# Optimization experiments

Measured on AMD Instinct MI355X. Metric: run time of the kernel, lower is better.

The kernel has to match this reference:

```python
import jax, jax.numpy as jnp
from jax import lax
import numpy as np

B, T = 256, 1024
LSTM_DIMS = [(64, 128), (256, 128), (256, 64)]  # (input, hidden) per layer


def setup_inputs() -> dict:
    key = jax.random.key(0)
    ks = jax.random.split(key, 32)
    s = 0.05
    p = {}
    p["x"] = jax.random.normal(ks[0], (B, 1, T), jnp.float32)
    p["conv_w"] = jax.random.normal(ks[1], (64, 1, 5), jnp.float32) * s  # OIW
    p["conv_b"] = jnp.zeros((64,), jnp.float32)
    for i, (D, H) in enumerate(LSTM_DIMS, 1):
        p[f"w_ih{i}"] = jax.random.normal(ks[3 * i], (2, 4 * H, D), jnp.float32) * s  # [dir, 4H, D]
        p[f"w_hh{i}"] = jax.random.normal(ks[3 * i + 1], (2, 4 * H, H), jnp.float32) * s
        p[f"b{i}"] = jnp.zeros((2, 4 * H), jnp.float32)  # b_ih + b_hh combined (equivalent math)
    fc_dims = [(512, 128), (256, 512), (128, 256), (2, 128)]
    for j, (O, I) in enumerate(fc_dims, 1):
        p[f"fc{j}_w"] = jax.random.normal(ks[12 + 2 * j], (O, I), jnp.float32) * s
        p[f"fc{j}_b"] = jnp.zeros((O,), jnp.float32)
    return p


def _lstm_dir(x, w_ih, w_hh, b, reverse):
    # x: [B,T,D] -> h: [B,T,H]; PyTorch gate order i,f,g,o
    Hh = w_hh.shape[1]
    xs = jnp.swapaxes(x, 0, 1)  # [T,B,D]
    if reverse:
        xs = xs[::-1]
    xw = jnp.einsum('tbd,gd->tbg', xs, w_ih) + b  # precompute input GEMMs: [T,B,4H]

    def step(carry, xw_t):
        h, c = carry
        gates = xw_t + h @ w_hh.T
        i, f, g, o = jnp.split(gates, 4, axis=-1)
        c = jax.nn.sigmoid(f) * c + jax.nn.sigmoid(i) * jnp.tanh(g)
        h = jax.nn.sigmoid(o) * jnp.tanh(c)
        return (h, c), h

    Bx = x.shape[0]
    init = (jnp.zeros((Bx, Hh), x.dtype), jnp.zeros((Bx, Hh), x.dtype))
    _, hs = lax.scan(step, init, xw)
    if reverse:
        hs = hs[::-1]
    return jnp.swapaxes(hs, 0, 1)  # [B,T,H]


def _bilstm(x, w_ih, w_hh, b):
    hf = _lstm_dir(x, w_ih[0], w_hh[0], b[0], False)
    hb = _lstm_dir(x, w_ih[1], w_hh[1], b[1], True)
    return jnp.concatenate([hf, hb], axis=-1)


def reference(x, conv_w, conv_b, w_ih1, w_hh1, b1, w_ih2, w_hh2, b2,
              w_ih3, w_hh3, b3, fc1_w, fc1_b, fc2_w, fc2_b, fc3_w, fc3_b, fc4_w, fc4_b):
    # causal conv: left-pad (k-1)=4, then VALID conv
    xp = jnp.pad(x, ((0, 0), (0, 0), (4, 0)))
    y = lax.conv_general_dilated(xp, conv_w, (1,), 'VALID',
                                 dimension_numbers=('NCH', 'OIH', 'NCH'))
    y = jax.nn.relu(y + conv_b[None, :, None]).transpose(0, 2, 1)  # [B,T,64]
    y = _bilstm(y, w_ih1, w_hh1, b1)  # [B,T,256]
    y = _bilstm(y, w_ih2, w_hh2, b2)  # [B,T,256]
    y = _bilstm(y, w_ih3, w_hh3, b3)  # [B,T,128]
    h = y[:, -1, :]  # [B,128]
    h = jax.nn.relu(h @ fc1_w.T + fc1_b)
    h = jax.nn.relu(h @ fc2_w.T + fc2_b)
    h = jax.nn.relu(h @ fc3_w.T + fc3_b)
    return h @ fc4_w.T + fc4_b  # [B,2]
```

## Files before the change

### kernel.cpp

```cpp
#include <hip/hip_runtime.h>
#include <hip/hip_bf16.h>
#include <cstdint>
#include <cstddef>

#define B_ALL 256
#define T_SZ  1024

typedef __attribute__((ext_vector_type(8))) _Float16  halfx8;
typedef __attribute__((ext_vector_type(4))) _Float16  halfx4;
typedef __attribute__((ext_vector_type(4))) float     f32x4;

__device__ __forceinline__ float sig_(float x) {
    return __builtin_amdgcn_rcpf(1.0f + __expf(-x));
}
__device__ __forceinline__ float tanh_(float x) {
    float ax = fabsf(x);
    float e  = __expf(-2.0f * ax);
    float t  = (1.0f - e) * __builtin_amdgcn_rcpf(1.0f + e);
    return copysignf(t, x);
}

__device__ __forceinline__ void bar_lgkm() {
    asm volatile("s_waitcnt lgkmcnt(0)\n\ts_barrier" ::: "memory");
}

__global__ void conv_relu_kernel(const float* __restrict__ x, const float* __restrict__ w,
                                 const float* __restrict__ bias, _Float16* __restrict__ out,
                                 int bg0)
{
    int c  = threadIdx.x & 63;
    int tq = threadIdx.x >> 6;
    int t  = blockIdx.x * 4 + tq;
    int b  = blockIdx.y;
    const float* xb = x + (size_t)(bg0 + b) * T_SZ;
    float s = bias[c];
#pragma unroll
    for (int k = 0; k < 5; ++k) {
        int ti = t - 4 + k;
        float xv = (ti >= 0) ? xb[ti] : 0.0f;
        s = fmaf(w[c * 5 + k], xv, s);
    }
    out[((size_t)b * T_SZ + t) * 64 + c] = (_Float16)fmaxf(s, 0.0f);
}

template <int H, int NW, bool WRITE_Y>
__global__ __launch_bounds__(512, 1) void fused_step(
    const _Float16* __restrict__ xwR, const float* __restrict__ w_hh,
    _Float16* __restrict__ y, float* __restrict__ lastOut,
    float* __restrict__ Hst, float* __restrict__ Cst,
    int Bg, int Tc, int lg, int step0, int zeroInit, int writeLast,
    int nRecBlocks, int ndirRec,
    const _Float16* __restrict__ A, const float* __restrict__ W,
    const float* __restrict__ bias, _Float16* __restrict__ xwOut,
    int K, int N, int t0p, int MT, int NT)
{
    __shared__ __align__(16) char smem[32768];
    const int tid = threadIdx.x;
    const int w   = tid >> 6;
    const int l   = tid & 63;
    const int l15 = l & 15;
    const int q4  = l >> 4;

    if ((int)blockIdx.x < nRecBlocks) {
        constexpr int FH  = 4 * H;
        constexpr int KT  = H / 32;
        constexpr int NCH = H / 8;
        int rb  = blockIdx.x;
        int dir = (ndirRec == 2) ? (rb & 1) : 0;
        int bt  = (ndirRec == 2) ? (rb >> 1) : rb;
        int brow = bt * 4 + q4;
        int hh   = w * 16 + l15;

        _Float16* hb = (_Float16*)smem;
        auto hAddr = [&](int p, int row, int ch) -> _Float16* {
            return hb + ((((p * 16 + row) * NCH) + (ch ^ (row & (NCH - 1)))) << 3);
        };
        for (int i = tid; i < 2 * 16 * NCH * 8; i += 512) hb[i] = (_Float16)0.f;
        __syncthreads();

        halfx8 wf[4][KT];
        float creg = 0.f;
        if (w < NW) {
            const float* wbase = w_hh + (size_t)dir * FH * H;
#pragma unroll
            for (int gate = 0; gate < 4; ++gate) {
                const float* wrow = wbase + (size_t)(gate * H + hh) * H;
#pragma unroll
                for (int kt = 0; kt < KT; ++kt) {
                    const float* src = wrow + kt * 32 + q4 * 8;
                    float4 a = *(const float4*)(src);
                    float4 b = *(const float4*)(src + 4);
                    halfx8 v;
                    v[0] = (_Float16)a.x; v[1] = (_Float16)a.y; v[2] = (_Float16)a.z; v[3] = (_Float16)a.w;
                    v[4] = (_Float16)b.x; v[5] = (_Float16)b.y; v[6] = (_Float16)b.z; v[7] = (_Float16)b.w;
                    wf[gate][kt] = v;
                }
            }
            float hv = 0.f;
            if (!zeroInit) {
                hv   = Hst[((size_t)dir * Bg + brow) * H + hh];
                creg = Cst[((size_t)dir * Bg + brow) * H + hh];
            }
            hAddr(0, q4 * 4, hh >> 3)[hh & 7] = (_Float16)hv;
        }
        const _Float16* xb = xwR + (size_t)dir * Tc * Bg * FH + (size_t)brow * FH + hh * 4;
        const size_t xstride = (size_t)Bg * FH;

        halfx4 pf0, pf1, pf2, pf3;
        if (w < NW) {
            pf0 = *(const halfx4*)(xb);
            pf1 = *(const halfx4*)(xb + xstride);
            pf2 = *(const halfx4*)(xb + 2 * xstride);
            pf3 = *(const halfx4*)(xb + 3 * xstride);
        }
        __syncthreads();

        auto step = [&](int sl, int P, halfx4 xv) {
            const int t = dir ? (T_SZ - 1 - (step0 + sl)) : (step0 + sl);
            halfx8 af[KT];
#pragma unroll
            for (int kt = 0; kt < KT; ++kt)
                af[kt] = *(const halfx8*)hAddr(P, l15, kt * 4 + q4);
            float g4[4];
#pragma unroll
            for (int gate = 0; gate < 4; ++gate) {
                f32x4 a = {0.f, 0.f, 0.f, 0.f};
#pragma unroll
                for (int kt = 0; kt < KT; ++kt)
                    a = __builtin_amdgcn_mfma_f32_16x16x32_f16(af[kt], wf[gate][kt], a, 0, 0, 0);
                g4[gate] = a[0] + (float)xv[gate];
            }
            float iv = fminf(fmaxf(g4[0], -25.f), 25.f);
            float fv = fminf(fmaxf(g4[1], -25.f), 25.f);
            float gv = fminf(fmaxf(g4[2], -12.f), 12.f);
            float ov = fminf(fmaxf(g4[3], -25.f), 25.f);
            float Af = 1.f + __expf(-fv);
            float Bi = 1.f + __expf(-iv);
            float G  = __expf(2.f * gv);
            float Gp = G + 1.f, Gm = G - 1.f;
            float num = fmaf(creg * Bi, Gp, Af * Gm);
            float cn  = num * __builtin_amdgcn_rcpf(Af * Bi * Gp);
            creg = cn;
            float cc = fminf(fmaxf(cn, -25.f), 25.f);
            float E  = __expf(2.f * cc);
            float hv = (E - 1.f) * __builtin_amdgcn_rcpf((1.f + __expf(-ov)) * (E + 1.f));
            hAddr(1 - P, q4 * 4, hh >> 3)[hh & 7] = (_Float16)hv;
            if (WRITE_Y) {
                y[((size_t)brow * T_SZ + t) * (2 * H) + dir * H + hh] = (_Float16)hv;
            } else if (writeLast && sl == Tc - 1) {
                lastOut[brow * 128 + hh] = hv;
            }
            if (sl == Tc - 1) {
                Hst[((size_t)dir * Bg + brow) * H + hh] = hv;
                Cst[((size_t)dir * Bg + brow) * H + hh] = cn;
            }
        };

        for (int sl4 = 0; sl4 < Tc; sl4 += 4) {
            if (w < NW) {
                step(sl4 + 0, 0, pf0);
                if (sl4 + 4 < Tc) pf0 = *(const halfx4*)(xb + (size_t)(sl4 + 4) * xstride);
            }
            bar_lgkm();
            if (w < NW) {
                step(sl4 + 1, 1, pf1);
                if (sl4 + 5 < Tc) pf1 = *(const halfx4*)(xb + (size_t)(sl4 + 5) * xstride);
            }
            bar_lgkm();
            if (w < NW) {
                step(sl4 + 2, 0, pf2);
                if (sl4 + 6 < Tc) pf2 = *(const halfx4*)(xb + (size_t)(sl4 + 6) * xstride);
            }
            bar_lgkm();
            if (w < NW) {
                step(sl4 + 3, 1, pf3);
                if (sl4 + 7 < Tc) pf3 = *(const halfx4*)(xb + (size_t)(sl4 + 7) * xstride);
            }
            bar_lgkm();
        }
    } else {
        const int Tcp = 1 << lg;
        const int H4  = N >> 2;
        int pb   = blockIdx.x - nRecBlocks;
        int mi   = pb % MT;
        int rest = pb / MT;
        int ni   = rest % NT;
        int dir  = rest / NT;
        const float* Wd = W + (size_t)dir * N * K;
        const float* bd = bias + (size_t)dir * N;
        _Float16*    od = xwOut + (size_t)dir * Tcp * Bg * N;

        _Float16 (*As)[40] = (_Float16(*)[40])smem;
        _Float16 (*Ws)[40] = (_Float16(*)[40])(smem + 10240);

        const int m0 = mi * 128;
        const int n0 = ni * 128;
        const int wm = (w & 1) * 64;
        const int wn = (w >> 1) * 32;

        f32x4 acc[4][2];
#pragma unroll
        for (int i = 0; i < 4; i++)
#pragma unroll
            for (int j = 0; j < 2; j++) acc[i][j] = (f32x4){0.f, 0.f, 0.f, 0.f};

        for (int k0 = 0; k0 < K; k0 += 32) {
            {
                int row = tid >> 2;
                int ko  = (tid & 3) * 8;
                int m   = m0 + row;
                int bA  = m >> lg, tl = m & (Tcp - 1);
                int t   = dir ? (T_SZ - 1 - (t0p + tl)) : (t0p + tl);
                const _Float16* src = A + ((size_t)bA * T_SZ + t) * K + k0 + ko;
                *(halfx8*)&As[row][ko] = *(const halfx8*)src;
            }
#pragma unroll
            for (int pass = 0; pass < 2; ++pass) {
                int c2  = tid + pass * 512;
                int row = c2 >> 3;
                int ko  = (c2 & 7) * 4;
                int n_o = n0 + row;
                int nr  = (n_o & 3) * H4 + (n_o >> 2);
                float4 f = *(const float4*)&Wd[(size_t)nr * K + k0 + ko];
                halfx4 v;
                v[0] = (_Float16)f.x; v[1] = (_Float16)f.y; v[2] = (_Float16)f.z; v[3] = (_Float16)f.w;
                *(halfx4*)&Ws[row][ko] = v;
            }
            bar_lgkm();
            halfx8 af[4], bfr[2];
#pragma unroll
            for (int i = 0; i < 4; i++) af[i]  = *(const halfx8*)&As[wm + i * 16 + l15][q4 * 8];
#pragma unroll
            for (int j = 0; j < 2; j++) bfr[j] = *(const halfx8*)&Ws[wn + j * 16 + l15][q4 * 8];
#pragma unroll
            for (int i = 0; i < 4; i++)
#pragma unroll
                for (int j = 0; j < 2; j++)
                    acc[i][j] = __builtin_amdgcn_mfma_f32_16x16x32_f16(af[i], bfr[j], acc[i][j], 0, 0, 0);
            bar_lgkm();
        }

        _Float16 (*Ct)[128] = (_Float16(*)[128])smem;
#pragma unroll
        for (int i = 0; i < 4; i++) {
#pragma unroll
            for (int j = 0; j < 2; j++) {
                int o_l = wn + j * 16 + l15;
                int n_o = n0 + o_l;
                float bi = bd[(n_o & 3) * H4 + (n_o >> 2)];
#pragma unroll
                for (int r = 0; r < 4; r++)
                    Ct[wm + i * 16 + q4 * 4 + r][o_l] = (_Float16)(acc[i][j][r] + bi);
            }
        }
        bar_lgkm();
        {
            int row = tid >> 2;
            int seg = tid & 3;
            int m   = m0 + row;
            int bO  = m >> lg, tl = m & (Tcp - 1);
            _Float16* dst = od + ((size_t)tl * Bg + bO) * N + n0 + seg * 32;
            const _Float16* srcp = &Ct[row][seg * 32];
#pragma unroll
            for (int u = 0; u < 4; ++u)
                *(halfx8*)(dst + u * 8) = *(const halfx8*)(srcp + u * 8);
        }
    }
}

__global__ __launch_bounds__(256) void lstm3_bwd_kernel(
    const _Float16* __restrict__ y2, const float* __restrict__ w_ih3,
    const float* __restrict__ b3, float* __restrict__ H3)
{
    int b = blockIdx.x, g = threadIdx.x;
    __shared__ float xr[256];
    __shared__ float gsh[256];
    xr[g] = (float)y2[((size_t)b * T_SZ + (T_SZ - 1)) * 256 + g];
    __syncthreads();
    const float* wr = w_ih3 + (size_t)256 * 256 + (size_t)g * 256;
    float acc = b3[256 + g];
#pragma unroll 4
    for (int k = 0; k < 256; k++) acc = fmaf(wr[k], xr[k], acc);
    gsh[g] = acc;
    __syncthreads();
    if (g < 64) {
        float iv = gsh[g], gv = gsh[128 + g], ov = gsh[192 + g];
        float ct = sig_(iv) * tanh_(gv);
        float hv = sig_(ov) * tanh_(ct);
        H3[b * 128 + 64 + g] = hv;
    }
}

__global__ void fc_kernel(const float* __restrict__ in, const float* __restrict__ W,
                          const float* __restrict__ bias, float* __restrict__ out,
                          int K, int N, int doRelu)
{
    int b = blockIdx.x;
    int g = threadIdx.x;
    extern __shared__ float xr[];
    for (int i = g; i < K; i += blockDim.x) xr[i] = in[(size_t)b * K + i];
    __syncthreads();
    if (g < N) {
        const float* wr = W + (size_t)g * K;
        float acc = bias[g];
        for (int k = 0; k < K; k++) acc = fmaf(wr[k], xr[k], acc);
        if (doRelu) acc = fmaxf(acc, 0.f);
        out[(size_t)b * N + g] = acc;
    }
}

extern "C" void kernel_launch(void* const* d_in, const int* in_sizes, int n_in,
                              void* d_out, int out_size, void* d_ws, size_t ws_size,
                              hipStream_t stream)
{
    (void)in_sizes; (void)n_in; (void)out_size;
    const float* x      = (const float*)d_in[0];
    const float* conv_w = (const float*)d_in[1];
    const float* conv_b = (const float*)d_in[2];
    const float* w_ih1  = (const float*)d_in[3];
    const float* w_hh1  = (const float*)d_in[4];
    const float* b1     = (const float*)d_in[5];
    const float* w_ih2  = (const float*)d_in[6];
    const float* w_hh2  = (const float*)d_in[7];
    const float* b2     = (const float*)d_in[8];
    const float* w_ih3  = (const float*)d_in[9];
    const float* w_hh3  = (const float*)d_in[10];
    const float* b3     = (const float*)d_in[11];
    const float* fc1_w  = (const float*)d_in[12];
    const float* fc1_b  = (const float*)d_in[13];
    const float* fc2_w  = (const float*)d_in[14];
    const float* fc2_b  = (const float*)d_in[15];
    const float* fc3_w  = (const float*)d_in[16];
    const float* fc3_b  = (const float*)d_in[17];
    const float* fc4_w  = (const float*)d_in[18];
    const float* fc4_b  = (const float*)d_in[19];
    float* out = (float*)d_out;
    char*  base = (char*)d_ws;

    const size_t MB = 1ull << 20;

    auto need = [&](int s, int tc) -> size_t {
        size_t Bg = B_ALL / s;
        size_t YB = Bg * T_SZ * 256 * 2;
        size_t XW = (size_t)tc * Bg * 512 * 2 * 2;
        return 2 * YB + 2 * XW + 2 * MB;
    };

    int S = 8;
    for (int s : {1, 2, 4, 8}) {
        if (need(s, 32) <= ws_size) { S = s; break; }
    }
    int Tc = 32;
    while (Tc < 256 && need(S, Tc * 2) <= ws_size) Tc <<= 1;
    int lg = 0; while ((1 << lg) < Tc) lg++;
    int NC = T_SZ / Tc;

    int Bg = B_ALL / S;
    size_t YB  = (size_t)Bg * T_SZ * 256 * 2;
    size_t XWB = (size_t)Tc * Bg * 512 * 2 * 2;
    _Float16* Y1 = (_Float16*)base;
    _Float16* Y2 = (_Float16*)(base + YB);
    _Float16* X1 = Y2;
    _Float16* XW[2] = { (_Float16*)(base + 2 * YB), (_Float16*)(base + 2 * YB + XWB) };
    float* sm  = (float*)(base + 2 * YB + 2 * XWB);
    float* Hs = sm;
    float* Cs = Hs + 2 * Bg * 128;
    float* H3 = Cs + 2 * Bg * 128;
    float* F1 = H3 + Bg * 128;
    float* F2 = F1 + Bg * 512;
    float* F3 = F2 + Bg * 256;

    int MT = Bg * Tc / 128;

    for (int sp = 0; sp < S; ++sp) {
        int bg0 = sp * Bg;

        conv_relu_kernel<<<dim3(T_SZ / 4, Bg), 256, 0, stream>>>(x, conv_w, conv_b, X1, bg0);

        {
            int NT = 4, ndir = 2, Kl = 64, Nn = 512;
            int nProj = MT * NT * ndir, nRec = (Bg / 4) * ndir;
            fused_step<128, 8, true><<<nProj, 512, 0, stream>>>(
                XW[0], w_hh1, Y1, H3, Hs, Cs, Bg, Tc, lg, 0, 1, 0, 0, ndir,
                X1, w_ih1, b1, XW[0], Kl, Nn, 0, MT, NT);
            int par = 0;
            for (int ci = 0; ci < NC; ++ci) {
                int last = (ci == NC - 1);
                int grid = nRec + (last ? 0 : nProj);
                fused_step<128, 8, true><<<grid, 512, 0, stream>>>(
                    XW[par], w_hh1, Y1, H3, Hs, Cs, Bg, Tc, lg, ci * Tc, ci == 0, 0, nRec, ndir,
                    X1, w_ih1, b1, XW[1 - par], Kl, Nn, (ci + 1) * Tc, MT, NT);
                par ^= 1;
            }
        }
        {
            int NT = 4, ndir = 2, Kl = 256, Nn = 512;
            int nProj = MT * NT * ndir, nRec = (Bg / 4) * ndir;
            fused_step<128, 8, true><<<nProj, 512, 0, stream>>>(
                XW[0], w_hh2, Y2, H3, Hs, Cs, Bg, Tc, lg, 0, 1, 0, 0, ndir,
                Y1, w_ih2, b2, XW[0], Kl, Nn, 0, MT, NT);
            int par = 0;
            for (int ci = 0; ci < NC; ++ci) {
                int last = (ci == NC - 1);
                int grid = nRec + (last ? 0 : nProj);
                fused_step<128, 8, true><<<grid, 512, 0, stream>>>(
                    XW[par], w_hh2, Y2, H3, Hs, Cs, Bg, Tc, lg, ci * Tc, ci == 0, 0, nRec, ndir,
                    Y1, w_ih2, b2, XW[1 - par], Kl, Nn, (ci + 1) * Tc, MT, NT);
                par ^= 1;
            }
        }
        {
            int NT = 2, ndir = 1, Kl = 256, Nn = 256;
            int nProj = MT * NT * ndir, nRec = (Bg / 4) * ndir;
            fused_step<64, 4, false><<<nProj, 512, 0, stream>>>(
                XW[0], w_hh3, nullptr, H3, Hs, Cs, Bg, Tc, lg, 0, 1, 0, 0, ndir,
                Y2, w_ih3, b3, XW[0], Kl, Nn, 0, MT, NT);
            int par = 0;
            for (int ci = 0; ci < NC; ++ci) {
                int last = (ci == NC - 1);
                int grid = nRec + (last ? 0 : nProj);
                fused_step<64, 4, false><<<grid, 512, 0, stream>>>(
                    XW[par], w_hh3, nullptr, H3, Hs, Cs, Bg, Tc, lg, ci * Tc, ci == 0, last, nRec, ndir,
                    Y2, w_ih3, b3, XW[1 - par], Kl, Nn, (ci + 1) * Tc, MT, NT);
                par ^= 1;
            }
        }
        lstm3_bwd_kernel<<<Bg, 256, 0, stream>>>(Y2, w_ih3, b3, H3);

        fc_kernel<<<Bg, 512, 128 * 4, stream>>>(H3, fc1_w, fc1_b, F1, 128, 512, 1);
        fc_kernel<<<Bg, 256, 512 * 4, stream>>>(F1, fc2_w, fc2_b, F2, 512, 256, 1);
        fc_kernel<<<Bg, 128, 256 * 4, stream>>>(F2, fc3_w, fc3_b, F3, 256, 128, 1);
        fc_kernel<<<Bg, 64, 128 * 4, stream>>>(F3, fc4_w, fc4_b, out + (size_t)bg0 * 2, 128, 2, 0);
    }
}
```

Before: 3.674 ms.

## Use full 16-row MFMA tiles per recurrent block and persist projection blocks

Each recurrent block now handles 16 batch rows instead of 4, using all four rows of each MFMA accumulator. Previously only one accumulator element per lane was used, so three quarters of the MFMA output was discarded. This cuts recurrent block count by four. Projection GEMM blocks become persistent and loop over tiles, with the grid sized so recurrent plus projection blocks total 256, roughly one per CU. The trade-off is more pointwise gate work and more xw prefetch registers per lane, and fewer recurrent blocks running in parallel.

```diff
diff --git a/kernel.cpp b/kernel.cpp
--- a/kernel.cpp
+++ b/kernel.cpp
@@ -43,7 +43,58 @@
     out[((size_t)b * T_SZ + t) * 64 + c] = (_Float16)fmaxf(s, 0.0f);
 }
 
-template <int H, int NW, bool WRITE_Y>
+#define REC_STEP(SL, PP, JJ) do {                                                          \
+    const int t_ = dir ? (T_SZ - 1 - (step0 + (SL))) : (step0 + (SL));                     \
+    halfx8 af[KT];                                                                          \
+    _Pragma("unroll")                                                                       \
+    for (int kt = 0; kt < KT; ++kt)                                                         \
+        af[kt] = *(const halfx8*)hAddr((PP), l15, kt * 4 + q4);                             \
+    f32x4 acc_[4];                                                                          \
+    _Pragma("unroll")                                                                       \
+    for (int g_ = 0; g_ < 4; ++g_) {                                                        \
+        f32x4 a_ = {0.f, 0.f, 0.f, 0.f};                                                    \
+        _Pragma("unroll")                                                                   \
+        for (int kt = 0; kt < KT; ++kt)                                                     \
+            a_ = __builtin_amdgcn_mfma_f32_16x16x32_f16(af[kt], wf[g_][kt], a_, 0, 0, 0);   \
+        acc_[g_] = a_;                                                                      \
+    }                                                                                       \
+    _Pragma("unroll")                                                                       \
+    for (int r_ = 0; r_ < 4; ++r_) {                                                        \
+        int m_ = q4 * 4 + r_;                                                               \
+        int brow_ = b0 + m_;                                                                \
+        halfx4 xv_ = pf[(JJ)][r_];                                                          \
+        float iv = acc_[0][r_] + (float)xv_[0];                                             \
+        float fv = acc_[1][r_] + (float)xv_[1];                                             \
+        float gv = acc_[2][r_] + (float)xv_[2];                                             \
+        float ov = acc_[3][r_] + (float)xv_[3];                                             \
+        iv = fminf(fmaxf(iv, -25.f), 25.f);                                                 \
+        fv = fminf(fmaxf(fv, -25.f), 25.f);                                                 \
+        gv = fminf(fmaxf(gv, -12.f), 12.f);                                                 \
+        ov = fminf(fmaxf(ov, -25.f), 25.f);                                                 \
+        float Af = 1.f + __expf(-fv);                                                       \
+        float Bi = 1.f + __expf(-iv);                                                       \
+        float G  = __expf(2.f * gv);                                                        \
+        float Gp = G + 1.f, Gm = G - 1.f;                                                   \
+        float num = fmaf(creg[r_] * Bi, Gp, Af * Gm);                                       \
+        float cn  = num * __builtin_amdgcn_rcpf(Af * Bi * Gp);                              \
+        creg[r_] = cn;                                                                      \
+        float cc = fminf(fmaxf(cn, -25.f), 25.f);                                           \
+        float E  = __expf(2.f * cc);                                                        \
+        float hvv = (E - 1.f) * __builtin_amdgcn_rcpf((1.f + __expf(-ov)) * (E + 1.f));     \
+        hAddr(1 - (PP), m_, hh >> 3)[hh & 7] = (_Float16)hvv;                               \
+        if (WRITE_Y) {                                                                      \
+            y[((size_t)brow_ * T_SZ + t_) * (2 * H) + dir * H + hh] = (_Float16)hvv;        \
+        } else if (writeLast && (SL) == Tc - 1) {                                           \
+            lastOut[brow_ * 128 + hh] = hvv;                                                \
+        }                                                                                   \
+        if ((SL) == Tc - 1) {                                                               \
+            Hst[((size_t)dir * Bg + brow_) * H + hh] = hvv;                                 \
+            Cst[((size_t)dir * Bg + brow_) * H + hh] = cn;                                  \
+        }                                                                                   \
+    }                                                                                       \
+} while (0)
+
+template <int H, bool WRITE_Y>
 __global__ __launch_bounds__(512, 1) void fused_step(
     const _Float16* __restrict__ xwR, const float* __restrict__ w_hh,
     _Float16* __restrict__ y, float* __restrict__ lastOut,
@@ -52,7 +103,7 @@
     int nRecBlocks, int ndirRec,
     const _Float16* __restrict__ A, const float* __restrict__ W,
     const float* __restrict__ bias, _Float16* __restrict__ xwOut,
-    int K, int N, int t0p, int MT, int NT)
+    int K, int N, int t0p, int MT, int NT, int nProjB, int totTiles)
 {
     __shared__ __align__(16) char smem[32768];
     const int tid = threadIdx.x;
@@ -64,22 +115,23 @@
     if ((int)blockIdx.x < nRecBlocks) {
         constexpr int FH  = 4 * H;
         constexpr int KT  = H / 32;
+        constexpr int NW  = H / 16;
         constexpr int NCH = H / 8;
         int rb  = blockIdx.x;
         int dir = (ndirRec == 2) ? (rb & 1) : 0;
         int bt  = (ndirRec == 2) ? (rb >> 1) : rb;
-        int brow = bt * 4 + q4;
-        int hh   = w * 16 + l15;
+        int b0  = bt * 16;
+        int hh  = w * 16 + l15;
 
         _Float16* hb = (_Float16*)smem;
         auto hAddr = [&](int p, int row, int ch) -> _Float16* {
             return hb + ((((p * 16 + row) * NCH) + (ch ^ (row & (NCH - 1)))) << 3);
         };
-        for (int i = tid; i < 2 * 16 * NCH * 8; i += 512) hb[i] = (_Float16)0.f;
+        for (int i = tid; i < 2 * 16 * H; i += 512) hb[i] = (_Float16)0.f;
         __syncthreads();
 
         halfx8 wf[4][KT];
-        float creg = 0.f;
+        float creg[4] = {0.f, 0.f, 0.f, 0.f};
         if (w < NW) {
             const float* wbase = w_hh + (size_t)dir * FH * H;
 #pragma unroll
@@ -96,174 +148,160 @@
                     wf[gate][kt] = v;
                 }
             }
-            float hv = 0.f;
-            if (!zeroInit) {
-                hv   = Hst[((size_t)dir * Bg + brow) * H + hh];
-                creg = Cst[((size_t)dir * Bg + brow) * H + hh];
-            }
-            hAddr(0, q4 * 4, hh >> 3)[hh & 7] = (_Float16)hv;
-        }
-        const _Float16* xb = xwR + (size_t)dir * Tc * Bg * FH + (size_t)brow * FH + hh * 4;
-        const size_t xstride = (size_t)Bg * FH;
-
-        halfx4 pf0, pf1, pf2, pf3;
+#pragma unroll
+            for (int r = 0; r < 4; ++r) {
+                int m = q4 * 4 + r;
+                int brow = b0 + m;
+                float hv = 0.f, cv = 0.f;
+                if (!zeroInit) {
+                    hv = Hst[((size_t)dir * Bg + brow) * H + hh];
+                    cv = Cst[((size_t)dir * Bg + brow) * H + hh];
+                }
+                creg[r] = cv;
+                hAddr(0, m, hh >> 3)[hh & 7] = (_Float16)hv;
+            }
+        }
+        const _Float16* xb = xwR + (size_t)dir * Tc * Bg * FH + (size_t)b0 * FH + hh * 4;
+        const size_t xstr = (size_t)Bg * FH;
+
+        halfx4 pf[4][4];
         if (w < NW) {
-            pf0 = *(const halfx4*)(xb);
-            pf1 = *(const halfx4*)(xb + xstride);
-            pf2 = *(const halfx4*)(xb + 2 * xstride);
-            pf3 = *(const halfx4*)(xb + 3 * xstride);
+#pragma unroll
+            for (int j = 0; j < 4; ++j)
+#pragma unroll
+                for (int r = 0; r < 4; ++r)
+                    pf[j][r] = *(const halfx4*)(xb + (size_t)j * xstr + (q4 * 4 + r) * FH);
         }
         __syncthreads();
-
-        auto step = [&](int sl, int P, halfx4 xv) {
-            const int t = dir ? (T_SZ - 1 - (step0 + sl)) : (step0 + sl);
-            halfx8 af[KT];
-#pragma unroll
-            for (int kt = 0; kt < KT; ++kt)
-                af[kt] = *(const halfx8*)hAddr(P, l15, kt * 4 + q4);
-            float g4[4];
-#pragma unroll
-            for (int gate = 0; gate < 4; ++gate) {
-                f32x4 a = {0.f, 0.f, 0.f, 0.f};
-#pragma unroll
-                for (int kt = 0; kt < KT; ++kt)
-                    a = __builtin_amdgcn_mfma_f32_16x16x32_f16(af[kt], wf[gate][kt], a, 0, 0, 0);
-                g4[gate] = a[0] + (float)xv[gate];
-            }
-            float iv = fminf(fmaxf(g4[0], -25.f), 25.f);
-            float fv = fminf(fmaxf(g4[1], -25.f), 25.f);
-            float gv = fminf(fmaxf(g4[2], -12.f), 12.f);
-            float ov = fminf(fmaxf(g4[3], -25.f), 25.f);
-            float Af = 1.f + __expf(-fv);
-            float Bi = 1.f + __expf(-iv);
-            float G  = __expf(2.f * gv);
-            float Gp = G + 1.f, Gm = G - 1.f;
-            float num = fmaf(creg * Bi, Gp, Af * Gm);
-            float cn  = num * __builtin_amdgcn_rcpf(Af * Bi * Gp);
-            creg = cn;
-            float cc = fminf(fmaxf(cn, -25.f), 25.f);
-            float E  = __expf(2.f * cc);
-            float hv = (E - 1.f) * __builtin_amdgcn_rcpf((1.f + __expf(-ov)) * (E + 1.f));
-            hAddr(1 - P, q4 * 4, hh >> 3)[hh & 7] = (_Float16)hv;
-            if (WRITE_Y) {
-                y[((size_t)brow * T_SZ + t) * (2 * H) + dir * H + hh] = (_Float16)hv;
-            } else if (writeLast && sl == Tc - 1) {
-                lastOut[brow * 128 + hh] = hv;
-            }
-            if (sl == Tc - 1) {
-                Hst[((size_t)dir * Bg + brow) * H + hh] = hv;
-                Cst[((size_t)dir * Bg + brow) * H + hh] = cn;
-            }
-        };
 
         for (int sl4 = 0; sl4 < Tc; sl4 += 4) {
             if (w < NW) {
-                step(sl4 + 0, 0, pf0);
-                if (sl4 + 4 < Tc) pf0 = *(const halfx4*)(xb + (size_t)(sl4 + 4) * xstride);
+                REC_STEP(sl4 + 0, 0, 0);
+                if (sl4 + 4 < Tc) {
+#pragma unroll
+                    for (int r = 0; r < 4; ++r)
+                        pf[0][r] = *(const halfx4*)(xb + (size_t)(sl4 + 4) * xstr + (q4 * 4 + r) * FH);
+                }
             }
             bar_lgkm();
             if (w < NW) {
-                step(sl4 + 1, 1, pf1);
-                if (sl4 + 5 < Tc) pf1 = *(const halfx4*)(xb + (size_t)(sl4 + 5) * xstride);
+                REC_STEP(sl4 + 1, 1, 1);
+                if (sl4 + 5 < Tc) {
+#pragma unroll
+                    for (int r = 0; r < 4; ++r)
+                        pf[1][r] = *(const halfx4*)(xb + (size_t)(sl4 + 5) * xstr + (q4 * 4 + r) * FH);
+                }
             }
             bar_lgkm();
             if (w < NW) {
-                step(sl4 + 2, 0, pf2);
-                if (sl4 + 6 < Tc) pf2 = *(const halfx4*)(xb + (size_t)(sl4 + 6) * xstride);
+                REC_STEP(sl4 + 2, 0, 2);
+                if (sl4 + 6 < Tc) {
+#pragma unroll
+                    for (int r = 0; r < 4; ++r)
+                        pf[2][r] = *(const halfx4*)(xb + (size_t)(sl4 + 6) * xstr + (q4 * 4 + r) * FH);
+                }
             }
             bar_lgkm();
             if (w < NW) {
-                step(sl4 + 3, 1, pf3);
-                if (sl4 + 7 < Tc) pf3 = *(const halfx4*)(xb + (size_t)(sl4 + 7) * xstride);
+                REC_STEP(sl4 + 3, 1, 3);
+                if (sl4 + 7 < Tc) {
+#pragma unroll
+                    for (int r = 0; r < 4; ++r)
+                        pf[3][r] = *(const halfx4*)(xb + (size_t)(sl4 + 7) * xstr + (q4 * 4 + r) * FH);
+                }
             }
             bar_lgkm();
         }
     } else {
         const int Tcp = 1 << lg;
         const int H4  = N >> 2;
-        int pb   = blockIdx.x - nRecBlocks;
-        int mi   = pb % MT;
-        int rest = pb / MT;
-        int ni   = rest % NT;
-        int dir  = rest / NT;
-        const float* Wd = W + (size_t)dir * N * K;
-        const float* bd = bias + (size_t)dir * N;
-        _Float16*    od = xwOut + (size_t)dir * Tcp * Bg * N;
-
-        _Float16 (*As)[40] = (_Float16(*)[40])smem;
-        _Float16 (*Ws)[40] = (_Float16(*)[40])(smem + 10240);
-
-        const int m0 = mi * 128;
-        const int n0 = ni * 128;
-        const int wm = (w & 1) * 64;
-        const int wn = (w >> 1) * 32;
-
-        f32x4 acc[4][2];
-#pragma unroll
-        for (int i = 0; i < 4; i++)
-#pragma unroll
-            for (int j = 0; j < 2; j++) acc[i][j] = (f32x4){0.f, 0.f, 0.f, 0.f};
-
-        for (int k0 = 0; k0 < K; k0 += 32) {
+        int pb = blockIdx.x - nRecBlocks;
+
+        for (int tile = pb; tile < totTiles; tile += nProjB) {
+            int mi   = tile % MT;
+            int rest = tile / MT;
+            int ni   = rest % NT;
+            int dirp = rest / NT;
+            const float* Wd = W + (size_t)dirp * N * K;
+            const float* bd = bias + (size_t)dirp * N;
+            _Float16*    od = xwOut + (size_t)dirp * Tcp * Bg * N;
+
+            _Float16 (*As)[40] = (_Float16(*)[40])smem;
+            _Float16 (*Ws)[40] = (_Float16(*)[40])(smem + 10240);
+
+            const int m0 = mi * 128;
+            const int n0 = ni * 128;
+            const int wm = (w & 1) * 64;
+            const int wn = (w >> 1) * 32;
+
+            f32x4 acc[4][2];
+#pragma unroll
+            for (int i = 0; i < 4; i++)
+#pragma unroll
+                for (int j = 0; j < 2; j++) acc[i][j] = (f32x4){0.f, 0.f, 0.f, 0.f};
+
+            for (int k0 = 0; k0 < K; k0 += 32) {
+                {
+                    int row = tid >> 2;
+                    int ko  = (tid & 3) * 8;
+                    int m   = m0 + row;
+                    int bA  = m >> lg, tl = m & (Tcp - 1);
+                    int t   = dirp ? (T_SZ - 1 - (t0p + tl)) : (t0p + tl);
+                    const _Float16* src = A + ((size_t)bA * T_SZ + t) * K + k0 + ko;
+                    *(halfx8*)&As[row][ko] = *(const halfx8*)src;
+                }
+#pragma unroll
+                for (int pass = 0; pass < 2; ++pass) {
+                    int c2  = tid + pass * 512;
+                    int row = c2 >> 3;
+                    int ko  = (c2 & 7) * 4;
+                    int n_o = n0 + row;
+                    int nr  = (n_o & 3) * H4 + (n_o >> 2);
+                    float4 f = *(const float4*)&Wd[(size_t)nr * K + k0 + ko];
+                    halfx4 v;
+                    v[0] = (_Float16)f.x; v[1] = (_Float16)f.y; v[2] = (_Float16)f.z; v[3] = (_Float16)f.w;
+                    *(halfx4*)&Ws[row][ko] = v;
+                }
+                bar_lgkm();
+                halfx8 af[4], bfr[2];
+#pragma unroll
+                for (int i = 0; i < 4; i++) af[i]  = *(const halfx8*)&As[wm + i * 16 + l15][q4 * 8];
+#pragma unroll
+                for (int j = 0; j < 2; j++) bfr[j] = *(const halfx8*)&Ws[wn + j * 16 + l15][q4 * 8];
+#pragma unroll
+                for (int i = 0; i < 4; i++)
+#pragma unroll
+                    for (int j = 0; j < 2; j++)
+                        acc[i][j] = __builtin_amdgcn_mfma_f32_16x16x32_f16(af[i], bfr[j], acc[i][j], 0, 0, 0);
+                bar_lgkm();
+            }
+
+            _Float16 (*Ct)[128] = (_Float16(*)[128])smem;
+#pragma unroll
+            for (int i = 0; i < 4; i++) {
+#pragma unroll
+                for (int j = 0; j < 2; j++) {
+                    int o_l = wn + j * 16 + l15;
+                    int n_o = n0 + o_l;
+                    float bi = bd[(n_o & 3) * H4 + (n_o >> 2)];
+#pragma unroll
+                    for (int r = 0; r < 4; r++)
+                        Ct[wm + i * 16 + q4 * 4 + r][o_l] = (_Float16)(acc[i][j][r] + bi);
+                }
+            }
+            bar_lgkm();
             {
                 int row = tid >> 2;
-                int ko  = (tid & 3) * 8;
+                int seg = tid & 3;
                 int m   = m0 + row;
-                int bA  = m >> lg, tl = m & (Tcp - 1);
-                int t   = dir ? (T_SZ - 1 - (t0p + tl)) : (t0p + tl);
-                const _Float16* src = A + ((size_t)bA * T_SZ + t) * K + k0 + ko;
-                *(halfx8*)&As[row][ko] = *(const halfx8*)src;
-            }
-#pragma unroll
-            for (int pass = 0; pass < 2; ++pass) {
-                int c2  = tid + pass * 512;
-                int row = c2 >> 3;
-                int ko  = (c2 & 7) * 4;
-                int n_o = n0 + row;
-                int nr  = (n_o & 3) * H4 + (n_o >> 2);
-                float4 f = *(const float4*)&Wd[(size_t)nr * K + k0 + ko];
-                halfx4 v;
-                v[0] = (_Float16)f.x; v[1] = (_Float16)f.y; v[2] = (_Float16)f.z; v[3] = (_Float16)f.w;
-                *(halfx4*)&Ws[row][ko] = v;
-            }
-            bar_lgkm();
-            halfx8 af[4], bfr[2];
-#pragma unroll
-            for (int i = 0; i < 4; i++) af[i]  = *(const halfx8*)&As[wm + i * 16 + l15][q4 * 8];
-#pragma unroll
-            for (int j = 0; j < 2; j++) bfr[j] = *(const halfx8*)&Ws[wn + j * 16 + l15][q4 * 8];
-#pragma unroll
-            for (int i = 0; i < 4; i++)
-#pragma unroll
-                for (int j = 0; j < 2; j++)
-                    acc[i][j] = __builtin_amdgcn_mfma_f32_16x16x32_f16(af[i], bfr[j], acc[i][j], 0, 0, 0);
-            bar_lgkm();
-        }
-
-        _Float16 (*Ct)[128] = (_Float16(*)[128])smem;
-#pragma unroll
-        for (int i = 0; i < 4; i++) {
-#pragma unroll
-            for (int j = 0; j < 2; j++) {
-                int o_l = wn + j * 16 + l15;
-                int n_o = n0 + o_l;
-                float bi = bd[(n_o & 3) * H4 + (n_o >> 2)];
-#pragma unroll
-                for (int r = 0; r < 4; r++)
-                    Ct[wm + i * 16 + q4 * 4 + r][o_l] = (_Float16)(acc[i][j][r] + bi);
-            }
-        }
-        bar_lgkm();
-        {
-            int row = tid >> 2;
-            int seg = tid & 3;
-            int m   = m0 + row;
-            int bO  = m >> lg, tl = m & (Tcp - 1);
-            _Float16* dst = od + ((size_t)tl * Bg + bO) * N + n0 + seg * 32;
-            const _Float16* srcp = &Ct[row][seg * 32];
-#pragma unroll
-            for (int u = 0; u < 4; ++u)
-                *(halfx8*)(dst + u * 8) = *(const halfx8*)(srcp + u * 8);
+                int bO  = m >> lg, tl = m & (Tcp - 1);
+                _Float16* dst = od + ((size_t)tl * Bg + bO) * N + n0 + seg * 32;
+                const _Float16* srcp = &Ct[row][seg * 32];
+#pragma unroll
+                for (int u = 0; u < 4; ++u)
+                    *(halfx8*)(dst + u * 8) = *(const halfx8*)(srcp + u * 8);
+            }
+            bar_lgkm();
         }
     }
 }
@@ -379,49 +417,55 @@
 
         {
             int NT = 4, ndir = 2, Kl = 64, Nn = 512;
-            int nProj = MT * NT * ndir, nRec = (Bg / 4) * ndir;
-            fused_step<128, 8, true><<<nProj, 512, 0, stream>>>(
+            int nRec  = (Bg / 16) * ndir;
+            int nProjB = 256 - nRec;
+            int totT  = MT * NT * ndir;
+            fused_step<128, true><<<nProjB, 512, 0, stream>>>(
                 XW[0], w_hh1, Y1, H3, Hs, Cs, Bg, Tc, lg, 0, 1, 0, 0, ndir,
-                X1, w_ih1, b1, XW[0], Kl, Nn, 0, MT, NT);
+                X1, w_ih1, b1, XW[0], Kl, Nn, 0, MT, NT, nProjB, totT);
             int par = 0;
             for (int ci = 0; ci < NC; ++ci) {
                 int last = (ci == NC - 1);
-                int grid = nRec + (last ? 0 : nProj);
-                fused_step<128, 8, true><<<grid, 512, 0, stream>>>(
+                int grid = nRec + (last ? 0 : nProjB);
+                fused_step<128, true><<<grid, 512, 0, stream>>>(
                     XW[par], w_hh1, Y1, H3, Hs, Cs, Bg, Tc, lg, ci * Tc, ci == 0, 0, nRec, ndir,
-                    X1, w_ih1, b1, XW[1 - par], Kl, Nn, (ci + 1) * Tc, MT, NT);
+                    X1, w_ih1, b1, XW[1 - par], Kl, Nn, (ci + 1) * Tc, MT, NT, nProjB, totT);
                 par ^= 1;
             }
         }
         {
             int NT = 4, ndir = 2, Kl = 256, Nn = 512;
-            int nProj = MT * NT * ndir, nRec = (Bg / 4) * ndir;
-            fused_step<128, 8, true><<<nProj, 512, 0, stream>>>(
+            int nRec  = (Bg / 16) * ndir;
+            int nProjB = 256 - nRec;
+            int totT  = MT * NT * ndir;
+            fused_step<128, true><<<nProjB, 512, 0, stream>>>(
                 XW[0], w_hh2, Y2, H3, Hs, Cs, Bg, Tc, lg, 0, 1, 0, 0, ndir,
-                Y1, w_ih2, b2, XW[0], Kl, Nn, 0, MT, NT);
+                Y1, w_ih2, b2, XW[0], Kl, Nn, 0, MT, NT, nProjB, totT);
             int par = 0;
             for (int ci = 0; ci < NC; ++ci) {
                 int last = (ci == NC - 1);
-                int grid = nRec + (last ? 0 : nProj);
-                fused_step<128, 8, true><<<grid, 512, 0, stream>>>(
+                int grid = nRec + (last ? 0 : nProjB);
+                fused_step<128, true><<<grid, 512, 0, stream>>>(
                     XW[par], w_hh2, Y2, H3, Hs, Cs, Bg, Tc, lg, ci * Tc, ci == 0, 0, nRec, ndir,
-                    Y1, w_ih2, b2, XW[1 - par], Kl, Nn, (ci + 1) * Tc, MT, NT);
+                    Y1, w_ih2, b2, XW[1 - par], Kl, Nn, (ci + 1) * Tc, MT, NT, nProjB, totT);
                 par ^= 1;
             }
         }
         {
             int NT = 2, ndir = 1, Kl = 256, Nn = 256;
-            int nProj = MT * NT * ndir, nRec = (Bg / 4) * ndir;
-            fused_step<64, 4, false><<<nProj, 512, 0, stream>>>(
+            int nRec  = (Bg / 16) * ndir;
+            int nProjB = 256 - nRec;
+            int totT  = MT * NT * ndir;
+            fused_step<64, false><<<nProjB, 512, 0, stream>>>(
                 XW[0], w_hh3, nullptr, H3, Hs, Cs, Bg, Tc, lg, 0, 1, 0, 0, ndir,
-                Y2, w_ih3, b3, XW[0], Kl, Nn, 0, MT, NT);
+                Y2, w_ih3, b3, XW[0], Kl, Nn, 0, MT, NT, nProjB, totT);
             int par = 0;
             for (int ci = 0; ci < NC; ++ci) {
                 int last = (ci == NC - 1);
-                int grid = nRec + (last ? 0 : nProj);
-                fused_step<64, 4, false><<<grid, 512, 0, stream>>>(
+                int grid = nRec + (last ? 0 : nProjB);
+                fused_step<64, false><<<grid, 512, 0, stream>>>(
                     XW[par], w_hh3, nullptr, H3, Hs, Cs, Bg, Tc, lg, ci * Tc, ci == 0, last, nRec, ndir,
-                    Y2, w_ih3, b3, XW[1 - par], Kl, Nn, (ci + 1) * Tc, MT, NT);
+                    Y2, w_ih3, b3, XW[1 - par], Kl, Nn, (ci + 1) * Tc, MT, NT, nProjB, totT);
                 par ^= 1;
             }
         }
```

Measured after the change: 6.971 ms. +89.7%, slower.
